# Performance work log

Hardware: AMD Instinct MI355X
Metric: run time of the kernel (lower is better)

## Reference

```python
import math
import jax, jax.numpy as jnp
import numpy as np

B, T, C = 2, 2048, 2048
NQ, NKV, H = 16, 4, 128
EPS = 1e-6
ROPE_BASE = 5.0e6


def setup_inputs() -> dict:
    key = jax.random.key(0)
    ks = jax.random.split(key, 6)
    x = jax.random.normal(ks[0], (B, T, C), dtype=jnp.float32)
    s = 0.02
    Wq = jax.random.normal(ks[1], (C, NQ * H), dtype=jnp.float32) * s
    Wk = jax.random.normal(ks[2], (C, NKV * H), dtype=jnp.float32) * s
    Wv = jax.random.normal(ks[3], (C, NKV * H), dtype=jnp.float32) * s
    Wo = jax.random.normal(ks[4], (NQ * H, C), dtype=jnp.float32) * s
    q_norm_w = jnp.ones((H,), dtype=jnp.float32)
    k_norm_w = jnp.ones((H,), dtype=jnp.float32)
    # RoPE tables (seq_start = 0)
    inv_freq = 1.0 / (ROPE_BASE ** (jnp.arange(0, H, 2, dtype=jnp.float32) / H))
    t = jnp.arange(T, dtype=jnp.float32)
    freqs = jnp.einsum('i,j->ij', t, inv_freq)          # [T, H/2]
    emb = jnp.concatenate([freqs, freqs], axis=-1)       # [T, H]
    cos = jnp.cos(emb)
    sin = jnp.sin(emb)
    # additive causal mask (finite large negative to stay nan-free)
    causal = jnp.tril(jnp.ones((T, T), dtype=bool))
    attn_mask = jnp.where(causal, 0.0, -1e9).astype(jnp.float32)
    return {"x": x, "Wq": Wq, "Wk": Wk, "Wv": Wv, "Wo": Wo,
            "q_norm_w": q_norm_w, "k_norm_w": k_norm_w,
            "cos": cos, "sin": sin, "attn_mask": attn_mask}


def _rms_norm(x, w):
    # x: [..., H]
    var = jnp.mean(x * x, axis=-1, keepdims=True)
    return w * (x * jax.lax.rsqrt(var + EPS))


def _rotate_half(x):
    x1, x2 = jnp.split(x, 2, axis=-1)
    return jnp.concatenate([-x2, x1], axis=-1)


def reference(x, Wq, Wk, Wv, Wo, q_norm_w, k_norm_w, cos, sin, attn_mask):
    q = (x @ Wq).reshape(B, T, NQ, H)
    k = (x @ Wk).reshape(B, T, NKV, H)
    v = (x @ Wv).reshape(B, T, NKV, H)
    q = _rms_norm(q, q_norm_w)
    k = _rms_norm(k, k_norm_w)
    c = cos[None, :, None, :]  # [1,T,1,H]
    s = sin[None, :, None, :]
    q = q * c + _rotate_half(q) * s
    k = k * c + _rotate_half(k) * s
    rep = NQ // NKV
    k = jnp.repeat(k, rep, axis=2)  # [B,T,NQ,H]
    v = jnp.repeat(v, rep, axis=2)
    scores = jnp.einsum('bihd,bjhd->bhij', q, k) / math.sqrt(H)
    scores = scores + attn_mask[None, None, :, :]
    probs = jax.nn.softmax(scores, axis=-1)
    ctx = jnp.einsum('bhij,bjhd->bihd', probs, v).reshape(B, T, NQ * H)
    return ctx @ Wo
```

## Files before the change

### kernel.cpp

```cpp
#include <hip/hip_runtime.h>
#include <hip/hip_bf16.h>

#define B_   2
#define T_   2048
#define C_   2048
#define NQ_  16
#define NKV_ 4
#define H_   128

using bf16x8 = __attribute__((ext_vector_type(8))) short;
using f32x4  = __attribute__((ext_vector_type(4))) float;

__device__ __forceinline__ unsigned short f2bf(float f) {
    __hip_bfloat16 h = __float2bfloat16(f);
    union { __hip_bfloat16 h; unsigned short s; } c;
    c.h = h;
    return c.s;
}
__device__ __forceinline__ float bf2f(unsigned short s) {
    return __uint_as_float(((unsigned)s) << 16);
}
__device__ __forceinline__ bf16x8 pack8(float4 f0, float4 f1) {
    bf16x8 r;
    r[0] = (short)f2bf(f0.x); r[1] = (short)f2bf(f0.y);
    r[2] = (short)f2bf(f0.z); r[3] = (short)f2bf(f0.w);
    r[4] = (short)f2bf(f1.x); r[5] = (short)f2bf(f1.y);
    r[6] = (short)f2bf(f1.z); r[7] = (short)f2bf(f1.w);
    return r;
}

#define MFMA16(a, b, c) __builtin_amdgcn_mfma_f32_16x16x32_bf16(a, b, c, 0, 0, 0)

__global__ void transpose_cvt(const float* __restrict__ src,
                              unsigned short* __restrict__ dst,
                              int R, int Cc) {
    const int tc = Cc >> 6;
    const int r0 = (blockIdx.x / tc) * 64;
    const int c0 = (blockIdx.x % tc) * 64;
    __shared__ unsigned short Tl[64 * 65];
    const int tid = threadIdx.x;
#pragma unroll
    for (int it = 0; it < 16; ++it) {
        const int idx = it * 256 + tid;
        const int r = idx >> 6, c = idx & 63;
        Tl[c * 65 + r] = f2bf(src[(size_t)(r0 + r) * Cc + c0 + c]);
    }
    __syncthreads();
#pragma unroll
    for (int it = 0; it < 16; ++it) {
        const int idx = it * 256 + tid;
        const int c = idx >> 6, r = idx & 63;
        dst[(size_t)(c0 + c) * R + r0 + r] = Tl[c * 65 + r];
    }
}

#define LDP 40

template <bool A_BF, bool OUT_F32>
__global__ __launch_bounds__(256, 2) void gemm_bt(
    const void* __restrict__ Av,
    const unsigned short* __restrict__ Bt,
    void* __restrict__ Cqv,
    unsigned short* __restrict__ Ck,
    unsigned short* __restrict__ Cv,
    int M, int N, int K, int fused) {
    const int ntn = N >> 7;
    const int tm  = blockIdx.x / ntn;
    const int tn  = blockIdx.x % ntn;

    const int tid  = threadIdx.x;
    const int wv   = tid >> 6;
    const int lane = tid & 63;
    const int col  = lane & 15;
    const int quad = lane >> 4;
    const int wm   = (wv & 1) * 64;
    const int wn   = (wv >> 1) * 64;

    __shared__ unsigned short Al[128 * LDP];
    __shared__ unsigned short Bl[128 * LDP];

    f32x4 acc[4][4];
#pragma unroll
    for (int mt = 0; mt < 4; ++mt)
#pragma unroll
        for (int nt = 0; nt < 4; ++nt) acc[mt][nt] = (f32x4){0.f, 0.f, 0.f, 0.f};

    const int i1 = tid, i2 = tid + 256;
    const size_t aoff1 = (size_t)(tm * 128 + (i1 >> 2)) * K + (i1 & 3) * 8;
    const size_t aoff2 = (size_t)(tm * 128 + (i2 >> 2)) * K + (i2 & 3) * 8;
    const size_t boff1 = (size_t)(tn * 128 + (i1 >> 2)) * K + (i1 & 3) * 8;
    const size_t boff2 = (size_t)(tn * 128 + (i2 >> 2)) * K + (i2 & 3) * 8;
    unsigned short* Aw1 = Al + (i1 >> 2) * LDP + (i1 & 3) * 8;
    unsigned short* Aw2 = Al + (i2 >> 2) * LDP + (i2 & 3) * 8;
    unsigned short* Bw1 = Bl + (i1 >> 2) * LDP + (i1 & 3) * 8;
    unsigned short* Bw2 = Bl + (i2 >> 2) * LDP + (i2 & 3) * 8;

    const unsigned short* Ab16 = (const unsigned short*)Av;
    const float*          Af   = (const float*)Av;

    uint4  a1u, a2u, b1u, b2u;
    float4 a1lo, a1hi, a2lo, a2hi;

    auto loadAB = [&](int kk) {
        if constexpr (A_BF) {
            a1u = *(const uint4*)(Ab16 + aoff1 + kk);
            a2u = *(const uint4*)(Ab16 + aoff2 + kk);
        } else {
            a1lo = *(const float4*)(Af + aoff1 + kk);
            a1hi = *(const float4*)(Af + aoff1 + kk + 4);
            a2lo = *(const float4*)(Af + aoff2 + kk);
            a2hi = *(const float4*)(Af + aoff2 + kk + 4);
        }
        b1u = *(const uint4*)(Bt + boff1 + kk);
        b2u = *(const uint4*)(Bt + boff2 + kk);
    };

    loadAB(0);

    for (int k0 = 0; k0 < K; k0 += 32) {
        __syncthreads();
        if constexpr (A_BF) {
            *(uint4*)Aw1 = a1u;
            *(uint4*)Aw2 = a2u;
        } else {
            *(bf16x8*)Aw1 = pack8(a1lo, a1hi);
            *(bf16x8*)Aw2 = pack8(a2lo, a2hi);
        }
        *(uint4*)Bw1 = b1u;
        *(uint4*)Bw2 = b2u;
        __syncthreads();

        const int kn = (k0 + 32 < K) ? k0 + 32 : k0;
        loadAB(kn);

        bf16x8 af[4], bfv[4];
#pragma unroll
        for (int t = 0; t < 4; ++t) {
            af[t]  = *(const bf16x8*)(Al + (wm + t * 16 + col) * LDP + quad * 8);
            bfv[t] = *(const bf16x8*)(Bl + (wn + t * 16 + col) * LDP + quad * 8);
        }
#pragma unroll
        for (int mt = 0; mt < 4; ++mt)
#pragma unroll
            for (int nt = 0; nt < 4; ++nt)
                acc[mt][nt] = MFMA16(af[mt], bfv[nt], acc[mt][nt]);
    }

    const int nb = tn * 128;
    if constexpr (OUT_F32) {
        float* Co = (float*)Cqv;
#pragma unroll
        for (int mt = 0; mt < 4; ++mt)
#pragma unroll
            for (int nt = 0; nt < 4; ++nt)
#pragma unroll
                for (int r = 0; r < 4; ++r) {
                    const int row = tm * 128 + wm + mt * 16 + quad * 4 + r;
                    const int cc  = nb + wn + nt * 16 + col;
                    Co[(size_t)row * N + cc] = acc[mt][nt][r];
                }
    } else {
        unsigned short* Cb;
        int ldc, nc0;
        if (!fused)         { Cb = (unsigned short*)Cqv; ldc = N;    nc0 = nb;        }
        else if (nb < 2048) { Cb = (unsigned short*)Cqv; ldc = 2048; nc0 = nb;        }
        else if (nb < 2560) { Cb = Ck;                   ldc = 512;  nc0 = nb - 2048; }
        else                { Cb = Cv;                   ldc = 512;  nc0 = nb - 2560; }
#pragma unroll
        for (int mt = 0; mt < 4; ++mt)
#pragma unroll
            for (int nt = 0; nt < 4; ++nt)
#pragma unroll
                for (int r = 0; r < 4; ++r) {
                    const int row = tm * 128 + wm + mt * 16 + quad * 4 + r;
                    const int cc  = nc0 + wn + nt * 16 + col;
                    Cb[(size_t)row * ldc + cc] = f2bf(acc[mt][nt][r]);
                }
    }
}

__global__ void norm_rope(unsigned short* __restrict__ buf,
                          const float* __restrict__ w,
                          const float* __restrict__ cosb,
                          const float* __restrict__ sinb,
                          int nheads, float oscale) {
    const int idx = blockIdx.x;
    const int h   = idx % nheads;
    const int bt  = idx / nheads;
    const int t   = bt % T_;
    unsigned short* row = buf + ((size_t)bt * nheads + h) * H_;
    const int l = threadIdx.x;

    const float x0 = bf2f(row[l]);
    const float x1 = bf2f(row[l + 64]);
    float ss = x0 * x0 + x1 * x1;
#pragma unroll
    for (int off = 32; off; off >>= 1) ss += __shfl_xor(ss, off);
    const float r = rsqrtf(ss * (1.0f / 128.0f) + 1e-6f) * oscale;

    const float n0 = x0 * r * w[l];
    const float n1 = x1 * r * w[l + 64];
    const float c0 = cosb[t * H_ + l];
    const float c1 = cosb[t * H_ + l + 64];
    const float s0 = sinb[t * H_ + l];
    const float s1 = sinb[t * H_ + l + 64];

    row[l]      = f2bf(n0 * c0 - n1 * s0);
    row[l + 64] = f2bf(n1 * c1 + n0 * s1);
}

__global__ __launch_bounds__(256, 2) void flash_attn(
    const unsigned short* __restrict__ qbuf,
    const unsigned short* __restrict__ kbuf,
    const unsigned short* __restrict__ vbuf,
    unsigned short* __restrict__ ctx) {
    const int blk = blockIdx.x;
    const int lo  = blk & 15;
    const int bh  = blk >> 4;
    const int qt  = (bh & 16) ? (15 - lo) : lo;
    const int h   = bh & 15;
    const int b   = bh >> 4;
    const int kvh = h >> 2;

    const int tid  = threadIdx.x;
    const int wave = tid >> 6;
    const int lane = tid & 63;
    const int col  = lane & 15;
    const int quad = lane >> 4;

    const int qbase = qt * 128;
    const int w0    = qbase + wave * 32;

    __shared__ unsigned short Kl[64 * 128];
    __shared__ unsigned short Vt[128 * 72];
    __shared__ unsigned short Pl[4][32 * 72];
    __shared__ float alf[4][32];

    bf16x8 qf[2][4];
#pragma unroll
    for (int nt = 0; nt < 2; ++nt)
#pragma unroll
        for (int ks = 0; ks < 4; ++ks) {
            const size_t off =
                ((size_t)(b * T_ + w0 + nt * 16 + col) * NQ_ + h) * H_ + ks * 32 + quad * 8;
            qf[nt][ks] = *(const bf16x8*)(qbuf + off);
        }

    f32x4 O[2][8];
#pragma unroll
    for (int pt = 0; pt < 2; ++pt)
#pragma unroll
        for (int dt = 0; dt < 8; ++dt) O[pt][dt] = (f32x4){0.f, 0.f, 0.f, 0.f};
    float m_run[2] = {-3.0e38f, -3.0e38f};
    float l_run[2] = {0.f, 0.f};

    const int swb = (col & 7) << 4;
    unsigned short* Pw = Pl[wave];
    unsigned* Vw = (unsigned*)Vt;
    const int nch = 2 * qt + 2;

    uint4 ka[4], va[4];
    const size_t kvstride = (size_t)NKV_ * H_;

    auto issueK = [&](int j0) {
#pragma unroll
        for (int i = 0; i < 4; ++i) {
            const int row = wave * 16 + i * 4 + quad;
            ka[i] = *(const uint4*)(
                kbuf + ((size_t)(b * T_ + j0 + row) * NKV_ + kvh) * H_ +
                ((col ^ (row & 7)) << 3));
        }
    };
    auto issueV = [&](int j0) {
#pragma unroll
        for (int it = 0; it < 2; ++it) {
            const int idx = it * 256 + tid;
            const int kp  = idx & 31;
            const int dc  = idx >> 5;
            const size_t g0 = ((size_t)(b * T_ + j0 + 2 * kp) * NKV_ + kvh) * H_ + dc * 8;
            va[2 * it]     = *(const uint4*)(vbuf + g0);
            va[2 * it + 1] = *(const uint4*)(vbuf + g0 + kvstride);
        }
    };
    auto writeK = [&]() {
#pragma unroll
        for (int i = 0; i < 4; ++i) {
            const int row = wave * 16 + i * 4 + quad;
            *(uint4*)(Kl + row * 128 + col * 8) = ka[i];
        }
    };
    auto writeV = [&]() {
#pragma unroll
        for (int it = 0; it < 2; ++it) {
            const int idx = it * 256 + tid;
            const int kp  = idx & 31;
            const int dc  = idx >> 5;
            const uint4 v0 = va[2 * it];
            const uint4 v1 = va[2 * it + 1];
            const int wb = dc * 288 + kp;
            Vw[wb + 0 * 36] = (v0.x & 0xFFFFu) | (v1.x << 16);
            Vw[wb + 1 * 36] = (v0.x >> 16)     | (v1.x & 0xFFFF0000u);
            Vw[wb + 2 * 36] = (v0.y & 0xFFFFu) | (v1.y << 16);
            Vw[wb + 3 * 36] = (v0.y >> 16)     | (v1.y & 0xFFFF0000u);
            Vw[wb + 4 * 36] = (v0.z & 0xFFFFu) | (v1.z << 16);
            Vw[wb + 5 * 36] = (v0.z >> 16)     | (v1.z & 0xFFFF0000u);
            Vw[wb + 6 * 36] = (v0.w & 0xFFFFu) | (v1.w << 16);
            Vw[wb + 7 * 36] = (v0.w >> 16)     | (v1.w & 0xFFFF0000u);
        }
    };

    issueK(0);
    issueV(0);

    for (int c = 0; c < nch; ++c) {
        const int j0 = c * 64;
        __syncthreads();
        writeK();
        writeV();
        __syncthreads();

        if (c + 1 < nch) {
            issueK(j0 + 64);
            issueV(j0 + 64);
        }

        if (j0 > w0 + 31) continue;

        f32x4 St[4][2];
#pragma unroll
        for (int mt = 0; mt < 4; ++mt)
#pragma unroll
            for (int nt = 0; nt < 2; ++nt) St[mt][nt] = (f32x4){0.f, 0.f, 0.f, 0.f};
#pragma unroll
        for (int ks = 0; ks < 4; ++ks)
#pragma unroll
            for (int mt = 0; mt < 4; ++mt) {
                const bf16x8 kfrag = *(const bf16x8*)(
                    Kl + ((mt * 16 + col) << 7) + (((ks * 64 + quad * 16) ^ swb) >> 1));
                St[mt][0] = MFMA16(kfrag, qf[0][ks], St[mt][0]);
                St[mt][1] = MFMA16(kfrag, qf[1][ks], St[mt][1]);
            }

        const bool needmask = (j0 + 63 > w0);
        if (needmask) {
            const int ig0 = w0 + col;
#pragma unroll
            for (int mt = 0; mt < 4; ++mt)
#pragma unroll
                for (int r = 0; r < 4; ++r) {
                    const int key = j0 + mt * 16 + quad * 4 + r;
                    if (key > ig0)      St[mt][0][r] = -3.0e38f;
                    if (key > ig0 + 16) St[mt][1][r] = -3.0e38f;
                }
        }

        float rm[2];
#pragma unroll
        for (int nt = 0; nt < 2; ++nt) {
            float m0 = fmaxf(fmaxf(St[0][nt][0], St[0][nt][1]),
                             fmaxf(St[0][nt][2], St[0][nt][3]));
#pragma unroll
            for (int mt = 1; mt < 4; ++mt)
                m0 = fmaxf(m0, fmaxf(fmaxf(St[mt][nt][0], St[mt][nt][1]),
                                     fmaxf(St[mt][nt][2], St[mt][nt][3])));
            m0 = fmaxf(m0, __shfl_xor(m0, 16));
            m0 = fmaxf(m0, __shfl_xor(m0, 32));
            rm[nt] = m0;
        }

        const int defer = __all((rm[0] <= m_run[0] + 8.0f) && (rm[1] <= m_run[1] + 8.0f));
        if (!defer) {
            const float mn0 = fmaxf(m_run[0], rm[0]);
            const float mn1 = fmaxf(m_run[1], rm[1]);
            const float al0 = exp2f(m_run[0] - mn0);
            const float al1 = exp2f(m_run[1] - mn1);
            m_run[0] = mn0; m_run[1] = mn1;
            l_run[0] *= al0; l_run[1] *= al1;
            if (quad == 0) { alf[wave][col] = al0; alf[wave][col + 16] = al1; }
        }

        float ls0 = 0.f, ls1 = 0.f;
#pragma unroll
        for (int mt = 0; mt < 4; ++mt) {
            const float p0 = exp2f(St[mt][0][0] - m_run[0]);
            const float p1 = exp2f(St[mt][0][1] - m_run[0]);
            const float p2 = exp2f(St[mt][0][2] - m_run[0]);
            const float p3 = exp2f(St[mt][0][3] - m_run[0]);
            ls0 += (p0 + p1) + (p2 + p3);
            *(uint2*)(Pw + col * 72 + mt * 16 + quad * 4) =
                make_uint2((unsigned)f2bf(p0) | ((unsigned)f2bf(p1) << 16),
                           (unsigned)f2bf(p2) | ((unsigned)f2bf(p3) << 16));
            const float q0 = exp2f(St[mt][1][0] - m_run[1]);
            const float q1 = exp2f(St[mt][1][1] - m_run[1]);
            const float q2 = exp2f(St[mt][1][2] - m_run[1]);
            const float q3 = exp2f(St[mt][1][3] - m_run[1]);
            ls1 += (q0 + q1) + (q2 + q3);
            *(uint2*)(Pw + (col + 16) * 72 + mt * 16 + quad * 4) =
                make_uint2((unsigned)f2bf(q0) | ((unsigned)f2bf(q1) << 16),
                           (unsigned)f2bf(q2) | ((unsigned)f2bf(q3) << 16));
        }
        ls0 += __shfl_xor(ls0, 16); ls0 += __shfl_xor(ls0, 32);
        ls1 += __shfl_xor(ls1, 16); ls1 += __shfl_xor(ls1, 32);
        l_run[0] += ls0; l_run[1] += ls1;

        if (!defer) {
            const f32x4 a0 = *(const f32x4*)&alf[wave][quad * 4];
            const f32x4 a1 = *(const f32x4*)&alf[wave][quad * 4 + 16];
#pragma unroll
            for (int dt = 0; dt < 8; ++dt)
#pragma unroll
                for (int r = 0; r < 4; ++r) { O[0][dt][r] *= a0[r]; O[1][dt][r] *= a1[r]; }
        }

#pragma unroll
        for (int ks = 0; ks < 2; ++ks) {
            const bf16x8 pa0 = *(const bf16x8*)(Pw + col * 72 + ks * 32 + quad * 8);
            const bf16x8 pa1 = *(const bf16x8*)(Pw + (col + 16) * 72 + ks * 32 + quad * 8);
#pragma unroll
            for (int dt = 0; dt < 8; ++dt) {
                const bf16x8 vf = *(const bf16x8*)(Vt + (dt * 16 + col) * 72 + ks * 32 + quad * 8);
                O[0][dt] = MFMA16(pa0, vf, O[0][dt]);
                O[1][dt] = MFMA16(pa1, vf, O[1][dt]);
            }
        }
    }

    if (quad == 0) {
        alf[wave][col]      = 1.0f / l_run[0];
        alf[wave][col + 16] = 1.0f / l_run[1];
    }
    const f32x4 i0 = *(const f32x4*)&alf[wave][quad * 4];
    const f32x4 i1 = *(const f32x4*)&alf[wave][quad * 4 + 16];
#pragma unroll
    for (int pt = 0; pt < 2; ++pt)
#pragma unroll
        for (int r = 0; r < 4; ++r) {
            const float inv = pt ? i1[r] : i0[r];
            const int ig = w0 + pt * 16 + quad * 4 + r;
            unsigned short* op = ctx + ((size_t)(b * T_ + ig) * NQ_ + h) * H_;
#pragma unroll
            for (int dt = 0; dt < 8; ++dt)
                op[dt * 16 + col] = f2bf(O[pt][dt][r] * inv);
        }
}

extern "C" void kernel_launch(void* const* d_in, const int* in_sizes, int n_in,
                              void* d_out, int out_size, void* d_ws, size_t ws_size,
                              hipStream_t stream) {
    const float* x    = (const float*)d_in[0];
    const float* Wq   = (const float*)d_in[1];
    const float* Wk   = (const float*)d_in[2];
    const float* Wv   = (const float*)d_in[3];
    const float* Wo   = (const float*)d_in[4];
    const float* qnw  = (const float*)d_in[5];
    const float* knw  = (const float*)d_in[6];
    const float* cosb = (const float*)d_in[7];
    const float* sinb = (const float*)d_in[8];

    const int M = B_ * T_;
    unsigned short* ws  = (unsigned short*)d_ws;
    unsigned short* WqT = ws;
    unsigned short* WkT = WqT + (size_t)2048 * 2048;
    unsigned short* WvT = WkT + (size_t)512 * 2048;
    unsigned short* ctx = ws;
    unsigned short* q   = ws + (size_t)8388608;
    unsigned short* k   = ws + (size_t)16777216;
    unsigned short* v   = ws + (size_t)18874368;
    unsigned short* WoT = q;

    transpose_cvt<<<(2048 / 64) * (2048 / 64), 256, 0, stream>>>(Wq, WqT, 2048, 2048);
    transpose_cvt<<<(2048 / 64) * (512 / 64),  256, 0, stream>>>(Wk, WkT, 2048, 512);
    transpose_cvt<<<(2048 / 64) * (512 / 64),  256, 0, stream>>>(Wv, WvT, 2048, 512);

    gemm_bt<false, false><<<(M / 128) * (3072 / 128), 256, 0, stream>>>(
        (const void*)x, WqT, (void*)q, k, v, M, 3072, C_, 1);

    norm_rope<<<M * NQ_, 64, 0, stream>>>(q, qnw, cosb, sinb, NQ_, 0.12751743f);
    norm_rope<<<M * NKV_, 64, 0, stream>>>(k, knw, cosb, sinb, NKV_, 1.0f);

    flash_attn<<<512, 256, 0, stream>>>(q, k, v, ctx);

    transpose_cvt<<<(2048 / 64) * (2048 / 64), 256, 0, stream>>>(Wo, WoT, 2048, 2048);
    gemm_bt<true, true><<<(M / 128) * (C_ / 128), 256, 0, stream>>>(
        (const void*)ctx, WoT, d_out, nullptr, nullptr, M, C_, NQ_ * H_, 0);
}
```

Before: 420.0 us.

## Balance causal flash-attention work by pairing short and long query tiles per block

Flash attention now runs 256 blocks of 512 threads, each split into two 4-wave groups with their own K/V LDS buffers. One group processes a short query tile and then the second half of the keys for the matching long tile. The other group processes the first half of that long tile's keys, so every block runs exactly 17 key chunks. The two partial softmax results for the long tile are merged through LDS using the saved max and sum values. This removes the load imbalance of the causal mask, at the cost of a larger LDS footprint (one block per CU) and an extra merge step.

Result: faster. 396.2 us (-5.7%).

```diff
diff --git a/kernel.cpp b/kernel.cpp
--- a/kernel.cpp
+++ b/kernel.cpp
@@ -209,42 +209,49 @@
     row[l + 64] = f2bf(n1 * c1 + n0 * s1);
 }
 
-__global__ __launch_bounds__(256, 2) void flash_attn(
+__global__ __launch_bounds__(512, 2) void flash_attn(
     const unsigned short* __restrict__ qbuf,
     const unsigned short* __restrict__ kbuf,
     const unsigned short* __restrict__ vbuf,
     unsigned short* __restrict__ ctx) {
     const int blk = blockIdx.x;
-    const int lo  = blk & 15;
-    const int bh  = blk >> 4;
-    const int qt  = (bh & 16) ? (15 - lo) : lo;
-    const int h   = bh & 15;
-    const int b   = bh >> 4;
+    const int p   = blk & 7;
+    const int h   = (blk >> 3) & 15;
+    const int b   = blk >> 7;
     const int kvh = h >> 2;
+    const int qtB = 15 - p;
 
     const int tid  = threadIdx.x;
     const int wave = tid >> 6;
+    const int g    = wave >> 2;
+    const int gw   = wave & 3;
     const int lane = tid & 63;
     const int col  = lane & 15;
     const int quad = lane >> 4;
-
-    const int qbase = qt * 128;
-    const int w0    = qbase + wave * 32;
-
-    __shared__ unsigned short Kl[64 * 128];
-    __shared__ unsigned short Vt[128 * 72];
-    __shared__ unsigned short Pl[4][32 * 72];
-    __shared__ float alf[4][32];
+    const int gtid = gw * 64 + lane;
+
+    int w0 = (g ? qtB : p) * 128 + gw * 32;
+    const int ph1 = 2 * p + 2;
+
+    __shared__ __align__(16) unsigned char smem[109568];
+    unsigned short* Kg   = (unsigned short*)smem + g * 8192;
+    unsigned short* Vg   = (unsigned short*)(smem + 32768) + g * 9216;
+    unsigned short* Pw   = (unsigned short*)(smem + 69632) + wave * 2304;
+    float*          alfw = (float*)(smem + 106496) + wave * 32;
+    unsigned*       Vw   = (unsigned*)Vg;
 
     bf16x8 qf[2][4];
-#pragma unroll
-    for (int nt = 0; nt < 2; ++nt)
-#pragma unroll
-        for (int ks = 0; ks < 4; ++ks) {
-            const size_t off =
-                ((size_t)(b * T_ + w0 + nt * 16 + col) * NQ_ + h) * H_ + ks * 32 + quad * 8;
-            qf[nt][ks] = *(const bf16x8*)(qbuf + off);
-        }
+    auto loadQ = [&]() {
+#pragma unroll
+        for (int nt = 0; nt < 2; ++nt)
+#pragma unroll
+            for (int ks = 0; ks < 4; ++ks) {
+                const size_t off =
+                    ((size_t)(b * T_ + w0 + nt * 16 + col) * NQ_ + h) * H_ + ks * 32 + quad * 8;
+                qf[nt][ks] = *(const bf16x8*)(qbuf + off);
+            }
+    };
+    loadQ();
 
     f32x4 O[2][8];
 #pragma unroll
@@ -255,9 +262,6 @@
     float l_run[2] = {0.f, 0.f};
 
     const int swb = (col & 7) << 4;
-    unsigned short* Pw = Pl[wave];
-    unsigned* Vw = (unsigned*)Vt;
-    const int nch = 2 * qt + 2;
 
     uint4 ka[4], va[4];
     const size_t kvstride = (size_t)NKV_ * H_;
@@ -265,7 +269,7 @@
     auto issueK = [&](int j0) {
 #pragma unroll
         for (int i = 0; i < 4; ++i) {
-            const int row = wave * 16 + i * 4 + quad;
+            const int row = gw * 16 + i * 4 + quad;
             ka[i] = *(const uint4*)(
                 kbuf + ((size_t)(b * T_ + j0 + row) * NKV_ + kvh) * H_ +
                 ((col ^ (row & 7)) << 3));
@@ -274,7 +278,7 @@
     auto issueV = [&](int j0) {
 #pragma unroll
         for (int it = 0; it < 2; ++it) {
-            const int idx = it * 256 + tid;
+            const int idx = it * 256 + gtid;
             const int kp  = idx & 31;
             const int dc  = idx >> 5;
             const size_t g0 = ((size_t)(b * T_ + j0 + 2 * kp) * NKV_ + kvh) * H_ + dc * 8;
@@ -285,14 +289,14 @@
     auto writeK = [&]() {
 #pragma unroll
         for (int i = 0; i < 4; ++i) {
-            const int row = wave * 16 + i * 4 + quad;
-            *(uint4*)(Kl + row * 128 + col * 8) = ka[i];
+            const int row = gw * 16 + i * 4 + quad;
+            *(uint4*)(Kg + row * 128 + col * 8) = ka[i];
         }
     };
     auto writeV = [&]() {
 #pragma unroll
         for (int it = 0; it < 2; ++it) {
-            const int idx = it * 256 + tid;
+            const int idx = it * 256 + gtid;
             const int kp  = idx & 31;
             const int dc  = idx >> 5;
             const uint4 v0 = va[2 * it];
@@ -309,19 +313,54 @@
         }
     };
 
+    auto storeOut = [&]() {
+        if (quad == 0) {
+            alfw[col]      = 1.0f / l_run[0];
+            alfw[col + 16] = 1.0f / l_run[1];
+        }
+        const f32x4 i0 = *(const f32x4*)&alfw[quad * 4];
+        const f32x4 i1 = *(const f32x4*)&alfw[quad * 4 + 16];
+#pragma unroll
+        for (int pt = 0; pt < 2; ++pt)
+#pragma unroll
+            for (int r = 0; r < 4; ++r) {
+                const float inv = pt ? i1[r] : i0[r];
+                const int ig = w0 + pt * 16 + quad * 4 + r;
+                unsigned short* op = ctx + ((size_t)(b * T_ + ig) * NQ_ + h) * H_;
+#pragma unroll
+                for (int dt = 0; dt < 8; ++dt)
+                    op[dt * 16 + col] = f2bf(O[pt][dt][r] * inv);
+            }
+    };
+
+    auto chunk_of = [&](int i) { return g ? i : (i < ph1 ? i : i + 15 - 2 * p); };
+
     issueK(0);
     issueV(0);
 
-    for (int c = 0; c < nch; ++c) {
-        const int j0 = c * 64;
+    for (int i = 0; i < 17; ++i) {
+        const int j0 = chunk_of(i) * 64;
         __syncthreads();
         writeK();
         writeV();
         __syncthreads();
 
-        if (c + 1 < nch) {
-            issueK(j0 + 64);
-            issueV(j0 + 64);
+        if (i + 1 < 17) {
+            const int jn = chunk_of(i + 1) * 64;
+            issueK(jn);
+            issueV(jn);
+        }
+
+        if (g == 0 && i == ph1) {
+            storeOut();
+#pragma unroll
+            for (int pt = 0; pt < 2; ++pt)
+#pragma unroll
+                for (int dt = 0; dt < 8; ++dt) O[pt][dt] = (f32x4){0.f, 0.f, 0.f, 0.f};
+            m_run[0] = m_run[1] = -3.0e38f;
+            l_run[0] = l_run[1] = 0.f;
+            w0 = qtB * 128 + gw * 32;
+            loadQ();
         }
 
         if (j0 > w0 + 31) continue;
@@ -336,7 +375,7 @@
 #pragma unroll
             for (int mt = 0; mt < 4; ++mt) {
                 const bf16x8 kfrag = *(const bf16x8*)(
-                    Kl + ((mt * 16 + col) << 7) + (((ks * 64 + quad * 16) ^ swb) >> 1));
+                    Kg + ((mt * 16 + col) << 7) + (((ks * 64 + quad * 16) ^ swb) >> 1));
                 St[mt][0] = MFMA16(kfrag, qf[0][ks], St[mt][0]);
                 St[mt][1] = MFMA16(kfrag, qf[1][ks], St[mt][1]);
             }
@@ -376,7 +415,7 @@
             const float al1 = exp2f(m_run[1] - mn1);
             m_run[0] = mn0; m_run[1] = mn1;
             l_run[0] *= al0; l_run[1] *= al1;
-            if (quad == 0) { alf[wave][col] = al0; alf[wave][col + 16] = al1; }
+            if (quad == 0) { alfw[col] = al0; alfw[col + 16] = al1; }
         }
 
         float ls0 = 0.f, ls1 = 0.f;
@@ -404,8 +443,8 @@
         l_run[0] += ls0; l_run[1] += ls1;
 
         if (!defer) {
-            const f32x4 a0 = *(const f32x4*)&alf[wave][quad * 4];
-            const f32x4 a1 = *(const f32x4*)&alf[wave][quad * 4 + 16];
+            const f32x4 a0 = *(const f32x4*)&alfw[quad * 4];
+            const f32x4 a1 = *(const f32x4*)&alfw[quad * 4 + 16];
 #pragma unroll
             for (int dt = 0; dt < 8; ++dt)
 #pragma unroll
@@ -418,30 +457,59 @@
             const bf16x8 pa1 = *(const bf16x8*)(Pw + (col + 16) * 72 + ks * 32 + quad * 8);
 #pragma unroll
             for (int dt = 0; dt < 8; ++dt) {
-                const bf16x8 vf = *(const bf16x8*)(Vt + (dt * 16 + col) * 72 + ks * 32 + quad * 8);
+                const bf16x8 vf = *(const bf16x8*)(Vg + (dt * 16 + col) * 72 + ks * 32 + quad * 8);
                 O[0][dt] = MFMA16(pa0, vf, O[0][dt]);
                 O[1][dt] = MFMA16(pa1, vf, O[1][dt]);
             }
         }
     }
 
-    if (quad == 0) {
-        alf[wave][col]      = 1.0f / l_run[0];
-        alf[wave][col + 16] = 1.0f / l_run[1];
-    }
-    const f32x4 i0 = *(const f32x4*)&alf[wave][quad * 4];
-    const f32x4 i1 = *(const f32x4*)&alf[wave][quad * 4 + 16];
-#pragma unroll
-    for (int pt = 0; pt < 2; ++pt)
-#pragma unroll
-        for (int r = 0; r < 4; ++r) {
-            const float inv = pt ? i1[r] : i0[r];
-            const int ig = w0 + pt * 16 + quad * 4 + r;
-            unsigned short* op = ctx + ((size_t)(b * T_ + ig) * NQ_ + h) * H_;
+    __syncthreads();
+    float* mlA = (float*)(smem + 107520);
+    float* mlB = (float*)(smem + 108544);
+    if (g == 0) {
+        float* Of = (float*)smem + gw * 4096;
+        float* ml = mlA + gw * 64;
+        if (quad == 0) {
+            ml[2 * col]            = m_run[0]; ml[2 * col + 1]        = l_run[0];
+            ml[2 * (col + 16)]     = m_run[1]; ml[2 * (col + 16) + 1] = l_run[1];
+        }
+#pragma unroll
+        for (int pt = 0; pt < 2; ++pt)
 #pragma unroll
             for (int dt = 0; dt < 8; ++dt)
-                op[dt * 16 + col] = f2bf(O[pt][dt][r] * inv);
-        }
+#pragma unroll
+                for (int r = 0; r < 4; ++r)
+                    Of[(pt * 16 + quad * 4 + r) * 128 + dt * 16 + col] = O[pt][dt][r];
+    }
+    __syncthreads();
+    if (g == 1) {
+        float* Of = (float*)smem + gw * 4096;
+        float* mA = mlA + gw * 64;
+        float* mB = mlB + gw * 64;
+        if (quad == 0) {
+            mB[2 * col]            = m_run[0]; mB[2 * col + 1]        = l_run[0];
+            mB[2 * (col + 16)]     = m_run[1]; mB[2 * (col + 16) + 1] = l_run[1];
+        }
+#pragma unroll
+        for (int pt = 0; pt < 2; ++pt)
+#pragma unroll
+            for (int r = 0; r < 4; ++r) {
+                const int row = pt * 16 + quad * 4 + r;
+                const float mBv = mB[2 * row], lBv = mB[2 * row + 1];
+                const float mAv = mA[2 * row], lAv = mA[2 * row + 1];
+                const float m  = fmaxf(mAv, mBv);
+                const float aB = exp2f(mBv - m);
+                const float aA = exp2f(mAv - m);
+                const float inv = 1.0f / (lBv * aB + lAv * aA);
+                const int ig = w0 + row;
+                unsigned short* op = ctx + ((size_t)(b * T_ + ig) * NQ_ + h) * H_;
+#pragma unroll
+                for (int dt = 0; dt < 8; ++dt)
+                    op[dt * 16 + col] =
+                        f2bf((O[pt][dt][r] * aB + Of[row * 128 + dt * 16 + col] * aA) * inv);
+            }
+    }
 }
 
 extern "C" void kernel_launch(void* const* d_in, const int* in_sizes, int n_in,
@@ -478,7 +546,7 @@
     norm_rope<<<M * NQ_, 64, 0, stream>>>(q, qnw, cosb, sinb, NQ_, 0.12751743f);
     norm_rope<<<M * NKV_, 64, 0, stream>>>(k, knw, cosb, sinb, NKV_, 1.0f);
 
-    flash_attn<<<512, 256, 0, stream>>>(q, k, v, ctx);
+    flash_attn<<<256, 512, 0, stream>>>(q, k, v, ctx);
 
     transpose_cvt<<<(2048 / 64) * (2048 / 64), 256, 0, stream>>>(Wo, WoT, 2048, 2048);
     gemm_bt<true, true><<<(M / 128) * (C_ / 128), 256, 0, stream>>>(
```
